# Performance work log

Hardware: AMD Instinct MI355X
Metric: run time of the kernel (lower is better)

Reference implementation:

```python
import jax
import jax.numpy as jnp
import numpy as np

# Periodic-boundary copy indices on the padded 18x18 lattice (dst <- src).
# None of the sources is an earlier destination, so one batched gather/scatter is faithful.
DST_R = np.array([1,1,2,3,4,4,6,7,8,10,11,12,14,14,15,16,17,17,16,15,14,14,12,10,8,6,4,4,3,2])
DST_C = np.array([3,5,7,9,10,11,13,13,14,15,15,16,15,16,15,14,13,11,9,7,6,5,3,2,1,0,0,1,1,2])
SRC_R = np.array([13,13,14,15,16,16,6,7,8,10,11,12,2,2,3,4,5,5,4,3,2,2,12,10,8,6,16,16,15,14])
SRC_C = np.array([15,5,7,9,10,11,1,1,2,3,3,4,3,4,3,2,1,11,9,7,6,5,15,14,13,12,12,13,13,14])

# 4x4 kernel sparsity masks (5 taps each)
_UP = np.zeros((4,4), np.float32);    _UP[[0,0,1,2,2],[0,1,1,1,2]] = 1
_LEFT = np.zeros((4,4), np.float32);  _LEFT[[1,2,2,2,3],[1,0,1,2,1]] = 1
_RIGHT = np.zeros((4,4), np.float32); _RIGHT[[1,2,2,2,3],[1,1,2,3,3]] = 1

def _out_mask():
    m = np.ones((16,16), np.float32)
    for i in range(9):
        m[i, 7+i:16] = 0
    for i in range(7):
        m[9+i, 0:i+1] = 0
    m[0,4:7]=0; m[1,6:8]=0; m[2,8]=0; m[3,9]=0
    m[6,12]=0; m[7,13]=0; m[8,14]=0; m[9,14]=0; m[10,14]=0; m[11,15]=0
    m[13:,14:]=0; m[15,13]=0; m[15,7:9]=0; m[13,5]=0; m[14,6]=0
    m[8,0]=0; m[9,1]=0; m[7,0]=0; m[3,0]=0; m[0:3,0:2]=0; m[0,2]=0
    return m
OUT_MASK = _out_mask()

def _conv(x, w, b):
    # kernel 4, stride 2, no padding: [B,C,18,18] -> [B,O,8,8]
    y = jax.lax.conv_general_dilated(x, w, window_strides=(2,2), padding='VALID',
                                     dimension_numbers=('NCHW','OIHW','NCHW'))
    return y + b[None, :, None, None]

def setup_inputs() -> dict:
    key = jax.random.key(0)
    ks = jax.random.split(key, 7)
    B, C, O = 2048, 64, 64
    x = jax.random.normal(ks[0], (B, C, 16, 16), dtype=jnp.float32)
    w_up = jax.random.normal(ks[1], (O, C, 4, 4), dtype=jnp.float32) * 0.05
    b_up = jax.random.normal(ks[2], (O,), dtype=jnp.float32) * 0.05
    w_left = jax.random.normal(ks[3], (O, C, 4, 4), dtype=jnp.float32) * 0.05
    b_left = jax.random.normal(ks[4], (O,), dtype=jnp.float32) * 0.05
    w_right = jax.random.normal(ks[5], (O, C, 4, 4), dtype=jnp.float32) * 0.05
    b_right = jax.random.normal(ks[6], (O,), dtype=jnp.float32) * 0.05
    return {"x": x, "w_up": w_up, "b_up": b_up, "w_left": w_left,
            "b_left": b_left, "w_right": w_right, "b_right": b_right}

def reference(x, w_up, b_up, w_left, b_left, w_right, b_right):
    # 1) zero-pad to 18x18 and apply periodic-boundary indexed copies
    xp = jnp.pad(x, ((0,0),(0,0),(1,1),(1,1)))
    xp = xp.at[:, :, DST_R, DST_C].set(xp[:, :, SRC_R, SRC_C])
    # 2) masked directional convs [B,O,8,8]
    up = _conv(xp, w_up * jnp.asarray(_UP), b_up)
    left = _conv(xp, w_left * jnp.asarray(_LEFT), b_left)
    right = _conv(xp, w_right * jnp.asarray(_RIGHT), b_right)
    # 3) interleave into 16x16: even rows = (up | 0) interleaved cols,
    #    odd rows = (left | right) interleaved cols
    B, O = up.shape[0], up.shape[1]
    out = jnp.zeros((B, O, 16, 16), x.dtype)
    out = out.at[:, :, 0::2, 0::2].set(up)
    out = out.at[:, :, 1::2, 0::2].set(left)
    out = out.at[:, :, 1::2, 1::2].set(right)
    # 4) static zero-out of non-lattice sites
    return out * jnp.asarray(OUT_MASK)
```

## Files before the change

kernel.cpp:

```cpp
#include <hip/hip_runtime.h>
#include <stdint.h>
#include <stddef.h>

typedef __attribute__((ext_vector_type(4))) float    f32x4;
typedef __attribute__((ext_vector_type(2))) float    f32x2;
typedef __attribute__((ext_vector_type(4))) uint32_t u32x4;
typedef __attribute__((ext_vector_type(8))) __bf16   bf16x8;

#define CGS   5200
#define NFRAG 15360

__device__ __constant__ uint8_t TAPR[15] = {0,0,1,2,2, 1,2,2,2,3, 1,2,2,2,3};
__device__ __constant__ uint8_t TAPC[15] = {0,1,1,1,2, 1,0,1,2,1, 1,1,2,3,3};

__device__ __constant__ uint8_t PDR[30] = {1,1,2,3,4,4,6,7,8,10,11,12,14,14,15,16,17,17,16,15,14,14,12,10,8,6,4,4,3,2};
__device__ __constant__ uint8_t PDC[30] = {3,5,7,9,10,11,13,13,14,15,15,16,15,16,15,14,13,11,9,7,6,5,3,2,1,0,0,1,1,2};
__device__ __constant__ uint8_t PSR[30] = {13,13,14,15,16,16,6,7,8,10,11,12,2,2,3,4,5,5,4,3,2,2,12,10,8,6,16,16,15,14};
__device__ __constant__ uint8_t PSC[30] = {15,5,7,9,10,11,1,1,2,3,3,4,3,4,3,2,1,11,9,7,6,5,15,14,13,12,12,13,13,14};

__device__ __forceinline__ uint32_t pk2(float a, float b) {
    return (uint32_t)__builtin_bit_cast(uint16_t, (__bf16)a)
         | ((uint32_t)__builtin_bit_cast(uint16_t, (__bf16)b) << 16);
}

__global__ __launch_bounds__(256) void pack_w(const float* __restrict__ wu,
                                              const float* __restrict__ wl,
                                              const float* __restrict__ wr,
                                              uint16_t* __restrict__ pw) {
    int fid = blockIdx.x * 256 + threadIdx.x;
    if (fid >= NFRAG) return;
    int lane = fid & 63;
    int mt   = (fid >> 6) & 3;
    int kk   = (fid >> 8) & 1;
    int td   = fid >> 9;
    const float* w = (td < 5) ? wu : (td < 10) ? wl : wr;
    int o  = mt * 16 + (lane & 15);
    int cb = kk * 32 + (lane >> 4) * 8;
    int kr = TAPR[td], kc = TAPC[td];
    const float* src = w + ((size_t)o * 64 + cb) * 16 + kr * 4 + kc;
    uint32_t d[4];
#pragma unroll
    for (int p = 0; p < 4; ++p)
        d[p] = pk2(src[(2 * p) * 16], src[(2 * p + 1) * 16]);
    u32x4 v = {d[0], d[1], d[2], d[3]};
    *(u32x4*)(pw + (size_t)fid * 8) = v;
}

__device__ __forceinline__ int slotof(int r, int c) { return (c & 1) * 162 + r * 9 + (c >> 1); }

__global__ __launch_bounds__(256, 3) void kagome_main(const float* __restrict__ x,
                                                      const uint16_t* __restrict__ pw,
                                                      const float* __restrict__ bu,
                                                      const float* __restrict__ bl,
                                                      const float* __restrict__ br,
                                                      float* __restrict__ out) {
    __shared__ __align__(16) uint8_t lds[8 * CGS];
    const int tid = threadIdx.x;
    const int b   = blockIdx.x;

    {
        const float* xb = x + (size_t)b * 16384;
#pragma unroll
        for (int i = 0; i < 2; ++i) {
            const int t    = i * 256 + tid;
            const int cg   = t >> 6;
            const int quad = t & 63;
            const int r0   = quad >> 2;
            const int qc   = quad & 3;
            f32x4 v[8];
#pragma unroll
            for (int ch = 0; ch < 8; ++ch)
                v[ch] = *(const f32x4*)(xb + (cg * 8 + ch) * 256 + quad * 4);
            uint8_t* base = lds + cg * CGS;
#pragma unroll
            for (int e = 0; e < 4; ++e) {
                const int pc   = 4 * qc + e + 1;
                const int slot = slotof(r0 + 1, pc);
                u32x4 w = {pk2(v[0][e], v[1][e]), pk2(v[2][e], v[3][e]),
                           pk2(v[4][e], v[5][e]), pk2(v[6][e], v[7][e])};
                *(u32x4*)(base + slot * 16) = w;
            }
        }
        u32x4 z = {0, 0, 0, 0};
        for (int idx = tid; idx < 68 * 8; idx += 256) {
            int s = idx >> 3, cg = idx & 7;
            int r, c;
            if (s < 18)      { r = 0;  c = s; }
            else if (s < 36) { r = 17; c = s - 18; }
            else             { int k2 = s - 36; r = 1 + (k2 >> 1); c = (k2 & 1) * 17; }
            *(u32x4*)(lds + cg * CGS + slotof(r, c) * 16) = z;
        }
    }
    __syncthreads();
    if (tid < 240) {
        int pair = tid >> 3, cg = tid & 7;
        int sa = slotof(PSR[pair], PSC[pair]);
        int da = slotof(PDR[pair], PDC[pair]);
        u32x4 v = *(const u32x4*)(lds + cg * CGS + sa * 16);
        *(u32x4*)(lds + cg * CGS + da * 16) = v;
    }
    __syncthreads();

    const int l   = tid & 63;
    const int wid = tid >> 6;
    const int q   = l >> 4;
    const int io  = (l >> 3) & 1;
    const int j   = l & 7;

    f32x4 acc[3][4];
#pragma unroll
    for (int d2 = 0; d2 < 3; ++d2)
#pragma unroll
        for (int n2 = 0; n2 < 4; ++n2) acc[d2][n2] = (f32x4){0.f, 0.f, 0.f, 0.f};

    const int bbase = q * CGS + io * 288 + j * 16;
    const uint16_t* pwl = pw + (size_t)l * 8;

#pragma unroll
    for (int kk = 0; kk < 2; ++kk) {
        bf16x8 aw[15];
#pragma unroll
        for (int f2 = 0; f2 < 15; ++f2) {
            u32x4 t = *(const u32x4*)(pwl + (size_t)((f2 * 2 + kk) * 4 + wid) * 512);
            aw[f2] = __builtin_bit_cast(bf16x8, t);
        }
        const uint8_t* lb = lds + kk * (4 * CGS) + bbase;
#pragma unroll
        for (int nt = 0; nt < 4; ++nt) {
#define BRD(dr, dc) __builtin_bit_cast(bf16x8, *(const u32x4*)(lb + ((dc) & 1) * 2592 + (4 * nt + (dr)) * 144 + ((dc) >> 1) * 16))
            bf16x8 b00 = BRD(0, 0);
            acc[0][nt] = __builtin_amdgcn_mfma_f32_16x16x32_bf16(aw[0], b00, acc[0][nt], 0, 0, 0);
            bf16x8 b01 = BRD(0, 1);
            acc[0][nt] = __builtin_amdgcn_mfma_f32_16x16x32_bf16(aw[1], b01, acc[0][nt], 0, 0, 0);
            bf16x8 b11 = BRD(1, 1);
            acc[0][nt] = __builtin_amdgcn_mfma_f32_16x16x32_bf16(aw[2],  b11, acc[0][nt], 0, 0, 0);
            acc[1][nt] = __builtin_amdgcn_mfma_f32_16x16x32_bf16(aw[5],  b11, acc[1][nt], 0, 0, 0);
            acc[2][nt] = __builtin_amdgcn_mfma_f32_16x16x32_bf16(aw[10], b11, acc[2][nt], 0, 0, 0);
            bf16x8 b20 = BRD(2, 0);
            acc[1][nt] = __builtin_amdgcn_mfma_f32_16x16x32_bf16(aw[6],  b20, acc[1][nt], 0, 0, 0);
            bf16x8 b21 = BRD(2, 1);
            acc[0][nt] = __builtin_amdgcn_mfma_f32_16x16x32_bf16(aw[3],  b21, acc[0][nt], 0, 0, 0);
            acc[1][nt] = __builtin_amdgcn_mfma_f32_16x16x32_bf16(aw[7],  b21, acc[1][nt], 0, 0, 0);
            acc[2][nt] = __builtin_amdgcn_mfma_f32_16x16x32_bf16(aw[11], b21, acc[2][nt], 0, 0, 0);
            bf16x8 b22 = BRD(2, 2);
            acc[0][nt] = __builtin_amdgcn_mfma_f32_16x16x32_bf16(aw[4],  b22, acc[0][nt], 0, 0, 0);
            acc[1][nt] = __builtin_amdgcn_mfma_f32_16x16x32_bf16(aw[8],  b22, acc[1][nt], 0, 0, 0);
            acc[2][nt] = __builtin_amdgcn_mfma_f32_16x16x32_bf16(aw[12], b22, acc[2][nt], 0, 0, 0);
            bf16x8 b23 = BRD(2, 3);
            acc[2][nt] = __builtin_amdgcn_mfma_f32_16x16x32_bf16(aw[13], b23, acc[2][nt], 0, 0, 0);
            bf16x8 b31 = BRD(3, 1);
            acc[1][nt] = __builtin_amdgcn_mfma_f32_16x16x32_bf16(aw[9],  b31, acc[1][nt], 0, 0, 0);
            bf16x8 b33 = BRD(3, 3);
            acc[2][nt] = __builtin_amdgcn_mfma_f32_16x16x32_bf16(aw[14], b33, acc[2][nt], 0, 0, 0);
#undef BRD
        }
    }

    float bias0[4], bias1[4], bias2[4];
#pragma unroll
    for (int r = 0; r < 4; ++r) {
        int o = wid * 16 + q * 4 + r;
        bias0[r] = bu[o]; bias1[r] = bl[o]; bias2[r] = br[o];
    }

    constexpr uint32_t RM[16] = {0x0008, 0x003C, 0x00FC, 0x01FE, 0x07FF, 0x0FFF, 0x0FFF, 0x1FFE,
                                 0x3FFE, 0xBFFC, 0xBFFC, 0x7FF8, 0xFFF0, 0x3FC0, 0x3F80, 0x1E00};
    const int odd = j & 1;
#pragma unroll
    for (int nt = 0; nt < 4; ++nt) {
        const int row_e = 4 * nt + 2 * io;
        const uint32_t me = io ? RM[4 * nt + 2] : RM[4 * nt + 0];
        const uint32_t mo = io ? RM[4 * nt + 3] : RM[4 * nt + 1];
        const uint32_t be  = (me >> (2 * j)) & 1u;
        const uint32_t bo0 = (mo >> (2 * j)) & 1u;
        const uint32_t bo1 = (mo >> (2 * j + 1)) & 1u;
#pragma unroll
        for (int r = 0; r < 4; ++r) {
            int o = wid * 16 + q * 4 + r;
            float up = acc[0][nt][r] + bias0[r];
            float lf = acc[1][nt][r] + bias1[r];
            float rt = acc[2][nt][r] + bias2[r];
            up = be  ? up : 0.f;
            lf = bo0 ? lf : 0.f;
            rt = bo1 ? rt : 0.f;
            float up_o = __shfl_xor(up, 1);
            float lf_o = __shfl_xor(lf, 1);
            float rt_o = __shfl_xor(rt, 1);
            f32x4 v;
            v[0] = odd ? lf_o : up;
            v[1] = odd ? rt_o : 0.f;
            v[2] = odd ? lf   : up_o;
            v[3] = odd ? rt   : 0.f;
            float* p = out + (((size_t)b * 64 + o) * 256 + (row_e + odd) * 16 + 4 * (j >> 1));
            __builtin_nontemporal_store(v, (f32x4*)p);
        }
    }
}

extern "C" void kernel_launch(void* const* d_in, const int* in_sizes, int n_in,
                              void* d_out, int out_size, void* d_ws, size_t ws_size,
                              hipStream_t stream) {
    const float* x  = (const float*)d_in[0];
    const float* wu = (const float*)d_in[1];
    const float* bu = (const float*)d_in[2];
    const float* wl = (const float*)d_in[3];
    const float* bl = (const float*)d_in[4];
    const float* wr = (const float*)d_in[5];
    const float* br = (const float*)d_in[6];
    float* out   = (float*)d_out;
    uint16_t* pw = (uint16_t*)d_ws;

    int B = in_sizes[0] / 16384;
    pack_w<<<(NFRAG + 255) / 256, 256, 0, stream>>>(wu, wl, wr, pw);
    kagome_main<<<B, 256, 0, stream>>>(x, pw, bu, bl, br, out);
}
```

Measured before the change: 58.58 us.

## Split input staging into two halves and overlap second-half fixup with compute

```diff
diff --git a/kernel.cpp b/kernel.cpp
--- a/kernel.cpp
+++ b/kernel.cpp
@@ -3,11 +3,10 @@
 #include <stddef.h>
 
 typedef __attribute__((ext_vector_type(4))) float    f32x4;
-typedef __attribute__((ext_vector_type(2))) float    f32x2;
 typedef __attribute__((ext_vector_type(4))) uint32_t u32x4;
 typedef __attribute__((ext_vector_type(8))) __bf16   bf16x8;
 
-#define CGS   5200
+#define CGS   5248
 #define NFRAG 15360
 
 __device__ __constant__ uint8_t TAPR[15] = {0,0,1,2,2, 1,2,2,2,3, 1,2,2,2,3};
@@ -58,28 +57,30 @@
     const int tid = threadIdx.x;
     const int b   = blockIdx.x;
 
+    const int cgA  = tid >> 6;
+    const int quad = tid & 63;
+    const int r0   = quad >> 2;
+    const int qc   = quad & 3;
+
+    f32x4 vA[8], vB[8];
     {
-        const float* xb = x + (size_t)b * 16384;
-#pragma unroll
-        for (int i = 0; i < 2; ++i) {
-            const int t    = i * 256 + tid;
-            const int cg   = t >> 6;
-            const int quad = t & 63;
-            const int r0   = quad >> 2;
-            const int qc   = quad & 3;
-            f32x4 v[8];
-#pragma unroll
-            for (int ch = 0; ch < 8; ++ch)
-                v[ch] = *(const f32x4*)(xb + (cg * 8 + ch) * 256 + quad * 4);
-            uint8_t* base = lds + cg * CGS;
-#pragma unroll
-            for (int e = 0; e < 4; ++e) {
-                const int pc   = 4 * qc + e + 1;
-                const int slot = slotof(r0 + 1, pc);
-                u32x4 w = {pk2(v[0][e], v[1][e]), pk2(v[2][e], v[3][e]),
-                           pk2(v[4][e], v[5][e]), pk2(v[6][e], v[7][e])};
-                *(u32x4*)(base + slot * 16) = w;
-            }
+        const float* xb = x + (size_t)b * 16384 + quad * 4;
+#pragma unroll
+        for (int ch = 0; ch < 8; ++ch)
+            vA[ch] = *(const f32x4*)(xb + (cgA * 8 + ch) * 256);
+#pragma unroll
+        for (int ch = 0; ch < 8; ++ch)
+            vB[ch] = *(const f32x4*)(xb + ((cgA + 4) * 8 + ch) * 256);
+    }
+
+    {
+        uint8_t* base = lds + cgA * CGS;
+#pragma unroll
+        for (int e = 0; e < 4; ++e) {
+            const int slot = slotof(r0 + 1, 4 * qc + e + 1);
+            u32x4 w = {pk2(vA[0][e], vA[1][e]), pk2(vA[2][e], vA[3][e]),
+                       pk2(vA[4][e], vA[5][e]), pk2(vA[6][e], vA[7][e])};
+            *(u32x4*)(base + slot * 16) = w;
         }
         u32x4 z = {0, 0, 0, 0};
         for (int idx = tid; idx < 68 * 8; idx += 256) {
@@ -92,14 +93,29 @@
         }
     }
     __syncthreads();
-    if (tid < 240) {
-        int pair = tid >> 3, cg = tid & 7;
-        int sa = slotof(PSR[pair], PSC[pair]);
-        int da = slotof(PDR[pair], PDC[pair]);
-        u32x4 v = *(const u32x4*)(lds + cg * CGS + sa * 16);
-        *(u32x4*)(lds + cg * CGS + da * 16) = v;
+
+    if (tid < 120) {
+        int pair = tid >> 2, cg = tid & 3;
+        u32x4 v = *(const u32x4*)(lds + cg * CGS + slotof(PSR[pair], PSC[pair]) * 16);
+        *(u32x4*)(lds + cg * CGS + slotof(PDR[pair], PDC[pair]) * 16) = v;
+    }
+    {
+        uint8_t* base = lds + (cgA + 4) * CGS;
+#pragma unroll
+        for (int e = 0; e < 4; ++e) {
+            const int slot = slotof(r0 + 1, 4 * qc + e + 1);
+            u32x4 w = {pk2(vB[0][e], vB[1][e]), pk2(vB[2][e], vB[3][e]),
+                       pk2(vB[4][e], vB[5][e]), pk2(vB[6][e], vB[7][e])};
+            *(u32x4*)(base + slot * 16) = w;
+        }
     }
     __syncthreads();
+
+    if (tid < 120) {
+        int pair = tid >> 2, cg = 4 + (tid & 3);
+        u32x4 v = *(const u32x4*)(lds + cg * CGS + slotof(PSR[pair], PSC[pair]) * 16);
+        *(u32x4*)(lds + cg * CGS + slotof(PDR[pair], PDC[pair]) * 16) = v;
+    }
 
     const int l   = tid & 63;
     const int wid = tid >> 6;
@@ -154,6 +170,7 @@
             acc[2][nt] = __builtin_amdgcn_mfma_f32_16x16x32_bf16(aw[14], b33, acc[2][nt], 0, 0, 0);
 #undef BRD
         }
+        if (kk == 0) __syncthreads();
     }
 
     float bias0[4], bias1[4], bias2[4];
```

Measured after the change: 59.97 us. 1.02x slower.

## Split each batch image across two blocks by output row halves

Applied to the files above, without the earlier changes.

```diff
diff --git a/kernel.cpp b/kernel.cpp
--- a/kernel.cpp
+++ b/kernel.cpp
@@ -3,24 +3,32 @@
 #include <stddef.h>
 
 typedef __attribute__((ext_vector_type(4))) float    f32x4;
-typedef __attribute__((ext_vector_type(2))) float    f32x2;
 typedef __attribute__((ext_vector_type(4))) uint32_t u32x4;
 typedef __attribute__((ext_vector_type(8))) __bf16   bf16x8;
 
-#define CGS   5200
+#define CGS   2944
 #define NFRAG 15360
 
 __device__ __constant__ uint8_t TAPR[15] = {0,0,1,2,2, 1,2,2,2,3, 1,2,2,2,3};
 __device__ __constant__ uint8_t TAPC[15] = {0,1,1,1,2, 1,0,1,2,1, 1,1,2,3,3};
 
-__device__ __constant__ uint8_t PDR[30] = {1,1,2,3,4,4,6,7,8,10,11,12,14,14,15,16,17,17,16,15,14,14,12,10,8,6,4,4,3,2};
-__device__ __constant__ uint8_t PDC[30] = {3,5,7,9,10,11,13,13,14,15,15,16,15,16,15,14,13,11,9,7,6,5,3,2,1,0,0,1,1,2};
-__device__ __constant__ uint8_t PSR[30] = {13,13,14,15,16,16,6,7,8,10,11,12,2,2,3,4,5,5,4,3,2,2,12,10,8,6,16,16,15,14};
-__device__ __constant__ uint8_t PSC[30] = {15,5,7,9,10,11,1,1,2,3,3,4,3,4,3,2,1,11,9,7,6,5,15,14,13,12,12,13,13,14};
+__device__ __constant__ uint8_t NLC[2]      = {5, 7};
+__device__ __constant__ uint8_t LDL[2][7]   = {{6,7,8,8,6,0,0},        {0,2,3,4,4,2,0}};
+__device__ __constant__ uint8_t LDCc[2][7]  = {{13,13,14,1,0,0,0},     {14,15,15,16,3,2,1}};
+__device__ __constant__ uint8_t LSL[2][7]   = {{6,7,8,8,6,0,0},        {0,2,3,4,4,2,0}};
+__device__ __constant__ uint8_t LSC[2][7]   = {{1,1,2,13,12,0,0},      {2,3,3,4,15,14,13}};
+__device__ __constant__ uint8_t GDL[2][10]  = {{1,1,2,3,4,4,4,4,3,2},  {6,6,7,8,9,9,8,7,6,6}};
+__device__ __constant__ uint8_t GDCc[2][10] = {{3,5,7,9,10,11,0,1,1,2},{15,16,15,14,13,11,9,7,6,5}};
+__device__ __constant__ uint8_t GXR[2][10]  = {{12,12,13,14,15,15,15,15,14,13},{1,1,2,3,4,4,3,2,1,1}};
+__device__ __constant__ uint8_t GXC[2][10]  = {{14,4,6,8,9,10,11,12,12,13},    {2,3,2,1,0,10,8,6,5,4}};
 
 __device__ __forceinline__ uint32_t pk2(float a, float b) {
     return (uint32_t)__builtin_bit_cast(uint16_t, (__bf16)a)
          | ((uint32_t)__builtin_bit_cast(uint16_t, (__bf16)b) << 16);
+}
+
+__device__ __forceinline__ int slotb(int lr, int c) {
+    return (c & 1) * 1440 + lr * 144 + (c >> 1) * 16;
 }
 
 __global__ __launch_bounds__(256) void pack_w(const float* __restrict__ wu,
@@ -46,9 +54,7 @@
     *(u32x4*)(pw + (size_t)fid * 8) = v;
 }
 
-__device__ __forceinline__ int slotof(int r, int c) { return (c & 1) * 162 + r * 9 + (c >> 1); }
-
-__global__ __launch_bounds__(256, 3) void kagome_main(const float* __restrict__ x,
+__global__ __launch_bounds__(256, 6) void kagome_main(const float* __restrict__ x,
                                                       const uint16_t* __restrict__ pw,
                                                       const float* __restrict__ bu,
                                                       const float* __restrict__ bl,
@@ -56,48 +62,79 @@
                                                       float* __restrict__ out) {
     __shared__ __align__(16) uint8_t lds[8 * CGS];
     const int tid = threadIdx.x;
-    const int b   = blockIdx.x;
+    const int b   = blockIdx.x >> 1;
+    const int h   = blockIdx.x & 1;
+    const float* xb = x + (size_t)b * 16384;
+
+    const int qc = tid & 3;
+    const int cg = (tid >> 2) & 7;
+    const int r  = tid >> 5;
+    const int xr0 = 7 * h;
+
+    f32x4 v[8], v2[8];
+#pragma unroll
+    for (int ch = 0; ch < 8; ++ch)
+        v[ch] = *(const f32x4*)(xb + (cg * 8 + ch) * 256 + (xr0 + r) * 16 + qc * 4);
+    if (tid < 32) {
+        const int qc2 = tid & 3, cg2 = tid >> 2;
+#pragma unroll
+        for (int ch = 0; ch < 8; ++ch)
+            v2[ch] = *(const f32x4*)(xb + (cg2 * 8 + ch) * 256 + (xr0 + 8) * 16 + qc2 * 4);
+    }
+    const int NL = NLC[h];
+    const int cpair = tid >> 3, ccg = tid & 7;
+    float g[8];
+    if (cpair >= NL && cpair < NL + 10) {
+        const int gi = cpair - NL;
+        const float* gp = xb + (size_t)ccg * 8 * 256 + GXR[h][gi] * 16 + GXC[h][gi];
+#pragma unroll
+        for (int ch = 0; ch < 8; ++ch) g[ch] = gp[ch * 256];
+    }
 
     {
-        const float* xb = x + (size_t)b * 16384;
+        uint8_t* base = lds + cg * CGS;
+        const int lr = r + 1 - h;
+#pragma unroll
+        for (int e = 0; e < 4; ++e) {
+            const int c = 4 * qc + e + 1;
+            u32x4 w = {pk2(v[0][e], v[1][e]), pk2(v[2][e], v[3][e]),
+                       pk2(v[4][e], v[5][e]), pk2(v[6][e], v[7][e])};
+            *(u32x4*)(base + slotb(lr, c)) = w;
+        }
+        if (tid < 32) {
+            const int qc2 = tid & 3, cg2 = tid >> 2;
+            uint8_t* base2 = lds + cg2 * CGS;
+            const int lr2 = 9 - h;
+#pragma unroll
+            for (int e = 0; e < 4; ++e) {
+                const int c = 4 * qc2 + e + 1;
+                u32x4 w = {pk2(v2[0][e], v2[1][e]), pk2(v2[2][e], v2[3][e]),
+                           pk2(v2[4][e], v2[5][e]), pk2(v2[6][e], v2[7][e])};
+                *(u32x4*)(base2 + slotb(lr2, c)) = w;
+            }
+        }
+        u32x4 z = {0, 0, 0, 0};
 #pragma unroll
         for (int i = 0; i < 2; ++i) {
-            const int t    = i * 256 + tid;
-            const int cg   = t >> 6;
-            const int quad = t & 63;
-            const int r0   = quad >> 2;
-            const int qc   = quad & 3;
-            f32x4 v[8];
-#pragma unroll
-            for (int ch = 0; ch < 8; ++ch)
-                v[ch] = *(const f32x4*)(xb + (cg * 8 + ch) * 256 + quad * 4);
-            uint8_t* base = lds + cg * CGS;
-#pragma unroll
-            for (int e = 0; e < 4; ++e) {
-                const int pc   = 4 * qc + e + 1;
-                const int slot = slotof(r0 + 1, pc);
-                u32x4 w = {pk2(v[0][e], v[1][e]), pk2(v[2][e], v[3][e]),
-                           pk2(v[4][e], v[5][e]), pk2(v[6][e], v[7][e])};
-                *(u32x4*)(base + slot * 16) = w;
+            int idx = tid + 256 * i;
+            if (idx < 288) {
+                int s = idx >> 3, zcg = idx & 7;
+                int lr, c;
+                if (s < 18) { lr = h ? 9 : 0; c = s; }
+                else        { int k2 = s - 18; lr = (k2 >> 1) + (1 - h); c = (k2 & 1) * 17; }
+                *(u32x4*)(lds + zcg * CGS + slotb(lr, c)) = z;
             }
         }
-        u32x4 z = {0, 0, 0, 0};
-        for (int idx = tid; idx < 68 * 8; idx += 256) {
-            int s = idx >> 3, cg = idx & 7;
-            int r, c;
-            if (s < 18)      { r = 0;  c = s; }
-            else if (s < 36) { r = 17; c = s - 18; }
-            else             { int k2 = s - 36; r = 1 + (k2 >> 1); c = (k2 & 1) * 17; }
-            *(u32x4*)(lds + cg * CGS + slotof(r, c) * 16) = z;
-        }
     }
     __syncthreads();
-    if (tid < 240) {
-        int pair = tid >> 3, cg = tid & 7;
-        int sa = slotof(PSR[pair], PSC[pair]);
-        int da = slotof(PDR[pair], PDC[pair]);
-        u32x4 v = *(const u32x4*)(lds + cg * CGS + sa * 16);
-        *(u32x4*)(lds + cg * CGS + da * 16) = v;
+
+    if (cpair < NL) {
+        u32x4 w = *(const u32x4*)(lds + ccg * CGS + slotb(LSL[h][cpair], LSC[h][cpair]));
+        *(u32x4*)(lds + ccg * CGS + slotb(LDL[h][cpair], LDCc[h][cpair])) = w;
+    } else if (cpair < NL + 10) {
+        const int gi = cpair - NL;
+        u32x4 w = {pk2(g[0], g[1]), pk2(g[2], g[3]), pk2(g[4], g[5]), pk2(g[6], g[7])};
+        *(u32x4*)(lds + ccg * CGS + slotb(GDL[h][gi], GDCc[h][gi])) = w;
     }
     __syncthreads();
 
@@ -107,13 +144,12 @@
     const int io  = (l >> 3) & 1;
     const int j   = l & 7;
 
-    f32x4 acc[3][4];
+    f32x4 acc[3][2];
 #pragma unroll
     for (int d2 = 0; d2 < 3; ++d2)
 #pragma unroll
-        for (int n2 = 0; n2 < 4; ++n2) acc[d2][n2] = (f32x4){0.f, 0.f, 0.f, 0.f};
-
-    const int bbase = q * CGS + io * 288 + j * 16;
+        for (int n2 = 0; n2 < 2; ++n2) acc[d2][n2] = (f32x4){0.f, 0.f, 0.f, 0.f};
+
     const uint16_t* pwl = pw + (size_t)l * 8;
 
 #pragma unroll
@@ -124,75 +160,76 @@
             u32x4 t = *(const u32x4*)(pwl + (size_t)((f2 * 2 + kk) * 4 + wid) * 512);
             aw[f2] = __builtin_bit_cast(bf16x8, t);
         }
-        const uint8_t* lb = lds + kk * (4 * CGS) + bbase;
-#pragma unroll
-        for (int nt = 0; nt < 4; ++nt) {
-#define BRD(dr, dc) __builtin_bit_cast(bf16x8, *(const u32x4*)(lb + ((dc) & 1) * 2592 + (4 * nt + (dr)) * 144 + ((dc) >> 1) * 16))
+        const uint8_t* lb = lds + (kk * 4 + q) * CGS + io * 288 + j * 16;
+#pragma unroll
+        for (int ntl = 0; ntl < 2; ++ntl) {
+#define BRD(dr, dc) __builtin_bit_cast(bf16x8, *(const u32x4*)(lb + ((dc) & 1) * 1440 + (4 * ntl + (dr)) * 144 + ((dc) >> 1) * 16))
             bf16x8 b00 = BRD(0, 0);
-            acc[0][nt] = __builtin_amdgcn_mfma_f32_16x16x32_bf16(aw[0], b00, acc[0][nt], 0, 0, 0);
+            acc[0][ntl] = __builtin_amdgcn_mfma_f32_16x16x32_bf16(aw[0], b00, acc[0][ntl], 0, 0, 0);
             bf16x8 b01 = BRD(0, 1);
-            acc[0][nt] = __builtin_amdgcn_mfma_f32_16x16x32_bf16(aw[1], b01, acc[0][nt], 0, 0, 0);
+            acc[0][ntl] = __builtin_amdgcn_mfma_f32_16x16x32_bf16(aw[1], b01, acc[0][ntl], 0, 0, 0);
             bf16x8 b11 = BRD(1, 1);
-            acc[0][nt] = __builtin_amdgcn_mfma_f32_16x16x32_bf16(aw[2],  b11, acc[0][nt], 0, 0, 0);
-            acc[1][nt] = __builtin_amdgcn_mfma_f32_16x16x32_bf16(aw[5],  b11, acc[1][nt], 0, 0, 0);
-            acc[2][nt] = __builtin_amdgcn_mfma_f32_16x16x32_bf16(aw[10], b11, acc[2][nt], 0, 0, 0);
+            acc[0][ntl] = __builtin_amdgcn_mfma_f32_16x16x32_bf16(aw[2],  b11, acc[0][ntl], 0, 0, 0);
+            acc[1][ntl] = __builtin_amdgcn_mfma_f32_16x16x32_bf16(aw[5],  b11, acc[1][ntl], 0, 0, 0);
+            acc[2][ntl] = __builtin_amdgcn_mfma_f32_16x16x32_bf16(aw[10], b11, acc[2][ntl], 0, 0, 0);
             bf16x8 b20 = BRD(2, 0);
-            acc[1][nt] = __builtin_amdgcn_mfma_f32_16x16x32_bf16(aw[6],  b20, acc[1][nt], 0, 0, 0);
+            acc[1][ntl] = __builtin_amdgcn_mfma_f32_16x16x32_bf16(aw[6],  b20, acc[1][ntl], 0, 0, 0);
             bf16x8 b21 = BRD(2, 1);
-            acc[0][nt] = __builtin_amdgcn_mfma_f32_16x16x32_bf16(aw[3],  b21, acc[0][nt], 0, 0, 0);
-            acc[1][nt] = __builtin_amdgcn_mfma_f32_16x16x32_bf16(aw[7],  b21, acc[1][nt], 0, 0, 0);
-            acc[2][nt] = __builtin_amdgcn_mfma_f32_16x16x32_bf16(aw[11], b21, acc[2][nt], 0, 0, 0);
+            acc[0][ntl] = __builtin_amdgcn_mfma_f32_16x16x32_bf16(aw[3],  b21, acc[0][ntl], 0, 0, 0);
+            acc[1][ntl] = __builtin_amdgcn_mfma_f32_16x16x32_bf16(aw[7],  b21, acc[1][ntl], 0, 0, 0);
+            acc[2][ntl] = __builtin_amdgcn_mfma_f32_16x16x32_bf16(aw[11], b21, acc[2][ntl], 0, 0, 0);
             bf16x8 b22 = BRD(2, 2);
-            acc[0][nt] = __builtin_amdgcn_mfma_f32_16x16x32_bf16(aw[4],  b22, acc[0][nt], 0, 0, 0);
-            acc[1][nt] = __builtin_amdgcn_mfma_f32_16x16x32_bf16(aw[8],  b22, acc[1][nt], 0, 0, 0);
-            acc[2][nt] = __builtin_amdgcn_mfma_f32_16x16x32_bf16(aw[12], b22, acc[2][nt], 0, 0, 0);
+            acc[0][ntl] = __builtin_amdgcn_mfma_f32_16x16x32_bf16(aw[4],  b22, acc[0][ntl], 0, 0, 0);
+            acc[1][ntl] = __builtin_amdgcn_mfma_f32_16x16x32_bf16(aw[8],  b22, acc[1][ntl], 0, 0, 0);
+            acc[2][ntl] = __builtin_amdgcn_mfma_f32_16x16x32_bf16(aw[12], b22, acc[2][ntl], 0, 0, 0);
             bf16x8 b23 = BRD(2, 3);
-            acc[2][nt] = __builtin_amdgcn_mfma_f32_16x16x32_bf16(aw[13], b23, acc[2][nt], 0, 0, 0);
+            acc[2][ntl] = __builtin_amdgcn_mfma_f32_16x16x32_bf16(aw[13], b23, acc[2][ntl], 0, 0, 0);
             bf16x8 b31 = BRD(3, 1);
-            acc[1][nt] = __builtin_amdgcn_mfma_f32_16x16x32_bf16(aw[9],  b31, acc[1][nt], 0, 0, 0);
+            acc[1][ntl] = __builtin_amdgcn_mfma_f32_16x16x32_bf16(aw[9],  b31, acc[1][ntl], 0, 0, 0);
             bf16x8 b33 = BRD(3, 3);
-            acc[2][nt] = __builtin_amdgcn_mfma_f32_16x16x32_bf16(aw[14], b33, acc[2][nt], 0, 0, 0);
+            acc[2][ntl] = __builtin_amdgcn_mfma_f32_16x16x32_bf16(aw[14], b33, acc[2][ntl], 0, 0, 0);
 #undef BRD
         }
     }
 
     float bias0[4], bias1[4], bias2[4];
 #pragma unroll
-    for (int r = 0; r < 4; ++r) {
-        int o = wid * 16 + q * 4 + r;
-        bias0[r] = bu[o]; bias1[r] = bl[o]; bias2[r] = br[o];
+    for (int rr = 0; rr < 4; ++rr) {
+        int o = wid * 16 + q * 4 + rr;
+        bias0[rr] = bu[o]; bias1[rr] = bl[o]; bias2[rr] = br[o];
     }
 
     constexpr uint32_t RM[16] = {0x0008, 0x003C, 0x00FC, 0x01FE, 0x07FF, 0x0FFF, 0x0FFF, 0x1FFE,
                                  0x3FFE, 0xBFFC, 0xBFFC, 0x7FF8, 0xFFF0, 0x3FC0, 0x3F80, 0x1E00};
     const int odd = j & 1;
 #pragma unroll
-    for (int nt = 0; nt < 4; ++nt) {
+    for (int ntl = 0; ntl < 2; ++ntl) {
+        const int nt = 2 * h + ntl;
         const int row_e = 4 * nt + 2 * io;
-        const uint32_t me = io ? RM[4 * nt + 2] : RM[4 * nt + 0];
-        const uint32_t mo = io ? RM[4 * nt + 3] : RM[4 * nt + 1];
+        const uint32_t me = RM[4 * nt + 2 * io];
+        const uint32_t mo = RM[4 * nt + 2 * io + 1];
         const uint32_t be  = (me >> (2 * j)) & 1u;
         const uint32_t bo0 = (mo >> (2 * j)) & 1u;
         const uint32_t bo1 = (mo >> (2 * j + 1)) & 1u;
 #pragma unroll
-        for (int r = 0; r < 4; ++r) {
-            int o = wid * 16 + q * 4 + r;
-            float up = acc[0][nt][r] + bias0[r];
-            float lf = acc[1][nt][r] + bias1[r];
-            float rt = acc[2][nt][r] + bias2[r];
+        for (int rr = 0; rr < 4; ++rr) {
+            int o = wid * 16 + q * 4 + rr;
+            float up = acc[0][ntl][rr] + bias0[rr];
+            float lf = acc[1][ntl][rr] + bias1[rr];
+            float rt = acc[2][ntl][rr] + bias2[rr];
             up = be  ? up : 0.f;
             lf = bo0 ? lf : 0.f;
             rt = bo1 ? rt : 0.f;
             float up_o = __shfl_xor(up, 1);
             float lf_o = __shfl_xor(lf, 1);
             float rt_o = __shfl_xor(rt, 1);
-            f32x4 v;
-            v[0] = odd ? lf_o : up;
-            v[1] = odd ? rt_o : 0.f;
-            v[2] = odd ? lf   : up_o;
-            v[3] = odd ? rt   : 0.f;
+            f32x4 sv;
+            sv[0] = odd ? lf_o : up;
+            sv[1] = odd ? rt_o : 0.f;
+            sv[2] = odd ? lf   : up_o;
+            sv[3] = odd ? rt   : 0.f;
             float* p = out + (((size_t)b * 64 + o) * 256 + (row_e + odd) * 16 + 4 * (j >> 1));
-            __builtin_nontemporal_store(v, (f32x4*)p);
+            __builtin_nontemporal_store(sv, (f32x4*)p);
         }
     }
 }
@@ -212,5 +249,5 @@
 
     int B = in_sizes[0] / 16384;
     pack_w<<<(NFRAG + 255) / 256, 256, 0, stream>>>(wu, wl, wr, pw);
-    kagome_main<<<B, 256, 0, stream>>>(x, pw, bu, bl, br, out);
-}
+    kagome_main<<<B * 2, 256, 0, stream>>>(x, pw, bu, bl, br, out);
+}
```

After: 76.88 us. 31.2% more time.
